# Performance work log

Measured on AMD Instinct MI355X. Metric: run time of the kernel, lower is better.

The kernel has to match this reference:

```python
import jax, jax.numpy as jnp
import numpy as np

LOD = 64          # latent observation dim
LSD = 2 * LOD     # latent state dim
BW = 3            # bandwidth
NB = 15           # num basis
B = 4096          # batch
H = 64            # hidden units of coefficient net

# band-structure indices (static, computed once)
_mask = np.triu(np.ones((LOD, LOD), np.float32), -BW) * np.tril(np.ones((LOD, LOD), np.float32), BW)
IDX0, IDX1 = np.where(_mask == 1)
DIAG_IDX = np.where(IDX0 == IDX1)[0]
NE = IDX0.shape[0]  # = 436 for lod=64, bw=3


def setup_inputs() -> dict:
    key = jax.random.key(0)
    ks = jax.random.split(key, 20)
    inp = {
        'prior_mean': jax.random.normal(ks[0], (B, LSD), jnp.float32),
        'cov_u': jax.random.uniform(ks[1], (B, LOD), jnp.float32) + 0.1,
        'cov_l': jax.random.uniform(ks[2], (B, LOD), jnp.float32) + 0.1,
        'cov_s': 0.1 * jax.random.uniform(ks[3], (B, LOD), jnp.float32),
        'obs': jax.random.normal(ks[4], (B, LOD), jnp.float32),
        'obs_var': jax.random.uniform(ks[5], (B, LOD), jnp.float32) + 0.1,
        # coefficient net params (Linear(LSD,H)-Tanh-Linear(H,H)-Tanh-Linear(H,NB)-Softmax)
        'W1': 0.05 * jax.random.normal(ks[6], (H, LSD), jnp.float32),
        'b1': jnp.zeros((H,), jnp.float32),
        'W2': 0.05 * jax.random.normal(ks[7], (H, H), jnp.float32),
        'b2': jnp.zeros((H,), jnp.float32),
        'W3': 0.05 * jax.random.normal(ks[8], (NB, H), jnp.float32),
        'b3': jnp.zeros((NB,), jnp.float32),
    }
    # transition basis matrices, flat band entries [NB, NE]
    tm11 = 0.02 * jax.random.normal(ks[9], (NB, NE), jnp.float32)
    tm12 = 0.02 * jax.random.normal(ks[10], (NB, NE), jnp.float32)
    tm12 = tm12.at[:, DIAG_IDX].add(0.2)
    tm21 = 0.02 * jax.random.normal(ks[11], (NB, NE), jnp.float32)
    tm21 = tm21.at[:, DIAG_IDX].add(-0.2)
    tm22 = 0.02 * jax.random.normal(ks[12], (NB, NE), jnp.float32)
    inp['tm11_basis'] = tm11
    inp['tm12_basis'] = tm12
    inp['tm21_basis'] = tm21
    inp['tm22_basis'] = tm22
    # log transition noise, init at var_activation_inverse(0.1) = log(exp(0.1)-1)
    inp['log_trans_noise'] = jnp.full((1, LSD), np.log(np.exp(0.1) - 1.0), jnp.float32)
    return inp


def _bmv(mat, vec):
    return jnp.einsum('bij,bj->bi', mat, vec)


def _unflatten_tm(flat):
    # flat: [B, NE] -> banded [B, LOD, LOD]
    tm = jnp.zeros((flat.shape[0], LOD, LOD), flat.dtype)
    return tm.at[:, IDX0, IDX1].set(flat)


def reference(prior_mean, cov_u, cov_l, cov_s, obs, obs_var,
              W1, b1, W2, b2, W3, b3,
              tm11_basis, tm12_basis, tm21_basis, tm22_basis, log_trans_noise):
    # ---- update (Kalman-style, factorized diagonal covariance) ----
    denom = cov_u + obs_var
    q_upper = cov_u / denom
    q_lower = cov_s / denom
    residual = obs - prior_mean[:, :LOD]
    post_mean = prior_mean + jnp.concatenate([q_upper * residual, q_lower * residual], -1)
    covar_factor = 1.0 - q_upper
    post_cu = covar_factor * cov_u
    post_cl = cov_l - q_lower * cov_s
    post_cs = covar_factor * cov_s

    # ---- coefficient net: MLP + softmax -> basis mixing coefficients ----
    h = jnp.tanh(post_mean @ W1.T + b1)
    h = jnp.tanh(h @ W2.T + b2)
    coeff = jax.nn.softmax(h @ W3.T + b3, axis=-1)  # [B, NB]

    # ---- locally-linear transition model ----
    tm11_flat = jnp.einsum('bk,ke->be', coeff, tm11_basis).at[:, DIAG_IDX].add(1.0)
    tm12_flat = jnp.einsum('bk,ke->be', coeff, tm12_basis)
    tm21_flat = jnp.einsum('bk,ke->be', coeff, tm21_basis)
    tm22_flat = jnp.einsum('bk,ke->be', coeff, tm22_basis).at[:, DIAG_IDX].add(1.0)
    tm11 = _unflatten_tm(tm11_flat)
    tm12 = _unflatten_tm(tm12_flat)
    tm21 = _unflatten_tm(tm21_flat)
    tm22 = _unflatten_tm(tm22_flat)

    trans_cov = jnp.log(jnp.exp(log_trans_noise) + 1.0)  # var_activation (softplus)
    tcu = trans_cov[:, :LOD]
    tcl = trans_cov[:, LOD:]

    # ---- predict ----
    mu = post_mean[:, :LOD]
    ml = post_mean[:, LOD:]
    next_mean = jnp.concatenate([_bmv(tm11, mu) + _bmv(tm12, ml),
                                 _bmv(tm21, mu) + _bmv(tm22, ml)], -1)
    # dadat(A, d) = bmv(A^2, d); dadbt(A, d, B) = bmv(A*B, d)
    next_cu = (_bmv(jnp.square(tm11), post_cu) + 2.0 * _bmv(tm11 * tm12, post_cs)
               + _bmv(jnp.square(tm12), post_cl) + tcu)
    next_cl = (_bmv(jnp.square(tm21), post_cu) + 2.0 * _bmv(tm21 * tm22, post_cs)
               + _bmv(jnp.square(tm22), post_cl) + tcl)
    next_cs = (_bmv(tm21 * tm11, post_cu) + _bmv(tm22 * tm11, post_cs)
               + _bmv(tm21 * tm12, post_cs) + _bmv(tm22 * tm12, post_cl))

    return (post_mean, post_cu, post_cl, post_cs, next_mean, next_cu, next_cl, next_cs)
```

## Files before the change

### kernel.cpp

```cpp
#include <hip/hip_runtime.h>
#include <math.h>

#define O_PM   0
#define O_PCU  524288
#define O_PCL  786432
#define O_PCS  1048576
#define O_NM   1310720
#define O_NCU  1835008
#define O_NCL  2097152
#define O_NCS  2359296

#define TM_S   1748
#define L_W1   0
#define L_W2   4864
#define L_W3   7680
#define L_TM   0
#define L_BAST 13984
#define L_PMB  27968
#define L_H1   29184
#define L_H2   29888
#define L_COEF 30592
#define L_PMF  30752
#define L_CUF  32800
#define L_CLF  33824
#define L_CSF  34848
#define L_TOT  35872

typedef short s8v __attribute__((ext_vector_type(8)));
typedef short s4v __attribute__((ext_vector_type(4)));
typedef float f4v __attribute__((ext_vector_type(4)));

__device__ __forceinline__ unsigned pk2(float a, float b) {
    unsigned ua = __float_as_uint(a), ub = __float_as_uint(b);
    ua += 0x7fffu + ((ua >> 16) & 1u);
    ub += 0x7fffu + ((ub >> 16) & 1u);
    return (ua >> 16) | (ub & 0xffff0000u);
}
__device__ __forceinline__ unsigned short tobf(float a) {
    unsigned ua = __float_as_uint(a);
    ua += 0x7fffu + ((ua >> 16) & 1u);
    return (unsigned short)(ua >> 16);
}
__device__ __forceinline__ float frombf(unsigned short u) {
    return __uint_as_float(((unsigned)u) << 16);
}
__device__ __forceinline__ float lo16(unsigned w) { return __uint_as_float(w << 16); }
__device__ __forceinline__ float hi16(unsigned w) { return __uint_as_float(w & 0xffff0000u); }
__device__ __forceinline__ float frcp(float x) { return __builtin_amdgcn_rcpf(x); }
__device__ __forceinline__ float ftanh(float x) {
    float e = __expf(2.f * x);
    return 1.f - 2.f * frcp(e + 1.f);
}
#define SWZ(v, imm) __uint_as_float((unsigned)__builtin_amdgcn_ds_swizzle((int)__float_as_uint(v), imm))

#if __has_builtin(__builtin_amdgcn_mfma_f32_16x16x16_bf16)
#define MFMA16(A,B,C) __builtin_amdgcn_mfma_f32_16x16x16_bf16(A,B,C,0,0,0)
#elif __has_builtin(__builtin_amdgcn_mfma_f32_16x16x16bf16_1k)
#define MFMA16(A,B,C) __builtin_amdgcn_mfma_f32_16x16x16bf16_1k(A,B,C,0,0,0)
#else
#define MFMA16(A,B,C) (C)
#endif

#if __has_builtin(__builtin_amdgcn_s_setprio)
#define SETPRIO(n) __builtin_amdgcn_s_setprio(n)
#else
#define SETPRIO(n)
#endif

__global__ __launch_bounds__(1024, 4)
void rkn_kernel(const float* __restrict__ prior_mean,
                const float* __restrict__ cov_u,
                const float* __restrict__ cov_l,
                const float* __restrict__ cov_s,
                const float* __restrict__ obs,
                const float* __restrict__ obs_var,
                const float* __restrict__ W1,
                const float* __restrict__ b1,
                const float* __restrict__ W2,
                const float* __restrict__ b2,
                const float* __restrict__ W3,
                const float* __restrict__ b3,
                const float* __restrict__ tm11b,
                const float* __restrict__ tm12b,
                const float* __restrict__ tm21b,
                const float* __restrict__ tm22b,
                const float* __restrict__ ltn,
                float* __restrict__ out)
{
    __shared__ __align__(16) unsigned smem[L_TOT];

    const int tid  = threadIdx.x;
    const int wid  = tid >> 6;
    const int lane = tid & 63;
    const int lrow = lane & 15;
    const int lkg  = lane >> 4;

    {
#pragma unroll
        for (int it = 0; it < 2; ++it) {
            const int idx = it * 1024 + tid;
            const float4 v = ((const float4*)W1)[idx];
            const int j = idx >> 5, kq = idx & 31;
            unsigned* d = smem + (L_W1 + j * 76 + kq * 2);
            d[0] = pk2(v.x, v.y); d[1] = pk2(v.z, v.w);
        }
        {
            const int idx = tid;
            const float4 v = ((const float4*)W2)[idx];
            const int j = idx >> 4, kq = idx & 15;
            unsigned* d = smem + (L_W2 + j * 44 + kq * 2);
            d[0] = pk2(v.x, v.y); d[1] = pk2(v.z, v.w);
        }
        if (tid < 240) {
            const float4 v = ((const float4*)W3)[tid];
            const int j = tid >> 4, kq = tid & 15;
            unsigned* d = smem + (L_W3 + j * 44 + kq * 2);
            d[0] = pk2(v.x, v.y); d[1] = pk2(v.z, v.w);
        } else if (tid < 284) {
            smem[L_W3 + 15 * 44 + (tid - 240)] = 0u;
        }
    }

    if (tid < 512) {
        const int prow  = tid >> 5;
        const int pd    = (tid & 31) << 1;
        const int grow1 = blockIdx.x * 16 + prow;
        const float2 cu2 = *(const float2*)(cov_u   + grow1 * 64 + pd);
        const float2 cl2 = *(const float2*)(cov_l   + grow1 * 64 + pd);
        const float2 cs2 = *(const float2*)(cov_s   + grow1 * 64 + pd);
        const float2 ob2 = *(const float2*)(obs     + grow1 * 64 + pd);
        const float2 ov2 = *(const float2*)(obs_var + grow1 * 64 + pd);
        const float2 pu2 = *(const float2*)(prior_mean + grow1 * 128 + pd);
        const float2 pl2 = *(const float2*)(prior_mean + grow1 * 128 + 64 + pd);

        const float i0 = frcp(cu2.x + ov2.x), i1 = frcp(cu2.y + ov2.y);
        const float qu0 = cu2.x * i0, qu1 = cu2.y * i1;
        const float ql0 = cs2.x * i0, ql1 = cs2.y * i1;
        const float r0 = ob2.x - pu2.x, r1 = ob2.y - pu2.y;
        const float pmu0 = pu2.x + qu0 * r0, pmu1 = pu2.y + qu1 * r1;
        const float pml0 = pl2.x + ql0 * r0, pml1 = pl2.y + ql1 * r1;
        const float cf0 = 1.f - qu0, cf1 = 1.f - qu1;
        const float pcu0 = cf0 * cu2.x, pcu1 = cf1 * cu2.y;
        const float pcl0 = cl2.x - ql0 * cs2.x, pcl1 = cl2.y - ql1 * cs2.y;
        const float pcs0 = cf0 * cs2.x, pcs1 = cf1 * cs2.y;

        *(float2*)(out + O_PM  + grow1 * 128 + pd)      = make_float2(pmu0, pmu1);
        *(float2*)(out + O_PM  + grow1 * 128 + 64 + pd) = make_float2(pml0, pml1);
        *(float2*)(out + O_PCU + grow1 * 64 + pd) = make_float2(pcu0, pcu1);
        *(float2*)(out + O_PCL + grow1 * 64 + pd) = make_float2(pcl0, pcl1);
        *(float2*)(out + O_PCS + grow1 * 64 + pd) = make_float2(pcs0, pcs1);

        smem[L_PMB + prow * 76 + (pd >> 1)]      = pk2(pmu0, pmu1);
        smem[L_PMB + prow * 76 + 32 + (pd >> 1)] = pk2(pml0, pml1);
        *(float2*)((float*)(smem + L_PMF) + prow * 128 + pd)      = make_float2(pmu0, pmu1);
        *(float2*)((float*)(smem + L_PMF) + prow * 128 + 64 + pd) = make_float2(pml0, pml1);
        *(float2*)((float*)(smem + L_CUF) + prow * 64 + pd) = make_float2(pcu0, pcu1);
        *(float2*)((float*)(smem + L_CLF) + prow * 64 + pd) = make_float2(pcl0, pcl1);
        *(float2*)((float*)(smem + L_CSF) + prow * 64 + pd) = make_float2(pcs0, pcs1);
    }

    const float tcu = __logf(__expf(ltn[lane]) + 1.f);
    const float tcl = __logf(__expf(ltn[64 + lane]) + 1.f);

    __syncthreads();

    const int t2 = tid - 256;
    const int ms = t2 & 3;
    const float* bps = (ms == 0) ? tm11b : (ms == 1) ? tm12b : (ms == 2) ? tm21b : tm22b;

    if (wid < 4) {
        SETPRIO(1);
        const int w = wid;
        f4v acc = {0.f, 0.f, 0.f, 0.f};
#pragma unroll
        for (int s = 0; s < 4; ++s) {
            s8v a = *(const s8v*)(smem + L_PMB + lrow * 76 + s * 16 + lkg * 4);
            s8v b = *(const s8v*)(smem + L_W1 + (w * 16 + lrow) * 76 + s * 16 + lkg * 4);
            acc = __builtin_amdgcn_mfma_f32_16x16x32_bf16(a, b, acc, 0, 0, 0);
        }
        const float bc1 = b1[w * 16 + lrow];
        unsigned short* h1u = (unsigned short*)(smem + L_H1);
#pragma unroll
        for (int q = 0; q < 4; ++q)
            h1u[(lkg * 4 + q) * 88 + w * 16 + lrow] = tobf(ftanh(acc[q] + bc1));
        SETPRIO(0);
    } else {
#pragma unroll
        for (int kp = 0; kp < 3; ++kp)
#pragma unroll
            for (int c = 0; c < 3; ++c) {
                const int n = c * 768 + t2;
                if (n < 1744) {
                    const int e = n >> 2;
                    const float lo = bps[(2 * kp) * 436 + e];
                    const float hi = bps[(2 * kp + 1) * 436 + e];
                    smem[L_BAST + kp * TM_S + n] = pk2(lo, hi);
                }
            }
    }
    __syncthreads();

    if (wid < 4) {
        SETPRIO(1);
        const int w = wid;
        f4v acc = {0.f, 0.f, 0.f, 0.f};
#pragma unroll
        for (int s = 0; s < 2; ++s) {
            s8v a = *(const s8v*)(smem + L_H1 + lrow * 44 + s * 16 + lkg * 4);
            s8v b = *(const s8v*)(smem + L_W2 + (w * 16 + lrow) * 44 + s * 16 + lkg * 4);
            acc = __builtin_amdgcn_mfma_f32_16x16x32_bf16(a, b, acc, 0, 0, 0);
        }
        const float bc2 = b2[w * 16 + lrow];
        unsigned short* h2u = (unsigned short*)(smem + L_H2);
#pragma unroll
        for (int q = 0; q < 4; ++q)
            h2u[(lkg * 4 + q) * 88 + w * 16 + lrow] = tobf(ftanh(acc[q] + bc2));
        SETPRIO(0);
    } else {
#pragma unroll
        for (int kp = 3; kp < 6; ++kp)
#pragma unroll
            for (int c = 0; c < 3; ++c) {
                const int n = c * 768 + t2;
                if (n < 1744) {
                    const int e = n >> 2;
                    const float lo = bps[(2 * kp) * 436 + e];
                    const float hi = bps[(2 * kp + 1) * 436 + e];
                    smem[L_BAST + kp * TM_S + n] = pk2(lo, hi);
                }
            }
    }
    __syncthreads();

    if (wid == 0) {
        SETPRIO(1);
        f4v acc = {0.f, 0.f, 0.f, 0.f};
#pragma unroll
        for (int s = 0; s < 2; ++s) {
            s8v a = *(const s8v*)(smem + L_H2 + lrow * 44 + s * 16 + lkg * 4);
            s8v b = *(const s8v*)(smem + L_W3 + lrow * 44 + s * 16 + lkg * 4);
            acc = __builtin_amdgcn_mfma_f32_16x16x32_bf16(a, b, acc, 0, 0, 0);
        }
        const float bc3 = (lrow < 15) ? b3[lrow] : 0.f;
        unsigned short* cfu = (unsigned short*)(smem + L_COEF);
#pragma unroll
        for (int q = 0; q < 4; ++q) {
            const float lg = acc[q] + bc3;
            float v = (lrow < 15) ? lg : -1e30f;
            v = fmaxf(v, SWZ(v, 0x041F));
            v = fmaxf(v, SWZ(v, 0x081F));
            v = fmaxf(v, SWZ(v, 0x101F));
            v = fmaxf(v, SWZ(v, 0x201F));
            const float ex = (lrow < 15) ? __expf(lg - v) : 0.f;
            float ss = ex;
            ss += SWZ(ss, 0x041F);
            ss += SWZ(ss, 0x081F);
            ss += SWZ(ss, 0x101F);
            ss += SWZ(ss, 0x201F);
            cfu[(lkg * 4 + q) * 20 + lrow] = tobf(ex * frcp(ss));
        }
        SETPRIO(0);
    } else if (wid >= 4) {
#pragma unroll
        for (int kp = 6; kp < 8; ++kp)
#pragma unroll
            for (int c = 0; c < 3; ++c) {
                const int n = c * 768 + t2;
                if (n < 1744) {
                    const int e = n >> 2;
                    const float lo = bps[(2 * kp) * 436 + e];
                    const float hi = (kp < 7) ? bps[(2 * kp + 1) * 436 + e] : 0.f;
                    smem[L_BAST + kp * TM_S + n] = pk2(lo, hi);
                }
            }
    }
    __syncthreads();

    {
        unsigned short* tmu = (unsigned short*)(smem + L_TM);
        const s4v ca = *(const s4v*)(smem + L_COEF + lrow * 10 + lkg * 2);
#pragma unroll
        for (int i = 0; i < 7; ++i) {
            const int t = i * 16 + wid;
            if (t < 109) {
                const int nn = t * 16 + lrow;
                unsigned wpair[2];
                wpair[0] = smem[L_BAST + (lkg * 2    ) * TM_S + nn];
                wpair[1] = smem[L_BAST + (lkg * 2 + 1) * TM_S + nn];
                const s4v bb = *(const s4v*)wpair;
                f4v d = {0.f, 0.f, 0.f, 0.f};
                d = MFMA16(ca, bb, d);
#pragma unroll
                for (int q = 0; q < 4; ++q)
                    tmu[(lkg * 4 + q) * TM_S + nn] = tobf(d[q]);
            }
        }
    }
    __syncthreads();

    {
        const int i   = lane;
        const int jlo = (i - 3 > 0) ? (i - 3) : 0;
        const int ne  = ((i + 3 < 63) ? (i + 3) : 63) - jlo + 1;
        const int base = (i < 4)  ? (i * (i + 7)) / 2
                       : (i <= 61) ? (7 * i - 6)
                       : (i == 62) ? 427 : 432;
        const float* pmf = (const float*)(smem + L_PMF);
        const float* cuf = (const float*)(smem + L_CUF);
        const float* clf = (const float*)(smem + L_CLF);
        const float* csf = (const float*)(smem + L_CSF);
        const uint2* tmr = (const uint2*)smem;

        const int r  = wid;
        const int gr = blockIdx.x * 16 + r;
        float nmu = 0.f, nml = 0.f, ncu = 0.f, ncl = 0.f, ncs = 0.f;
#pragma unroll
        for (int dd = 0; dd < 7; ++dd) {
            if (dd < ne) {
                const int j = jlo + dd;
                const uint2 tv = tmr[r * (TM_S / 4) + base + dd];
                float t11 = lo16(tv.x);
                float t12 = hi16(tv.x);
                float t21 = lo16(tv.y);
                float t22 = hi16(tv.y);
                if (j == i) { t11 += 1.f; t22 += 1.f; }
                const float mu  = pmf[r * 128 + j];
                const float ml  = pmf[r * 128 + 64 + j];
                const float vcu = cuf[r * 64 + j];
                const float vcl = clf[r * 64 + j];
                const float vcs = csf[r * 64 + j];
                nmu += t11 * mu + t12 * ml;
                nml += t21 * mu + t22 * ml;
                ncu += t11 * t11 * vcu + 2.f * t11 * t12 * vcs + t12 * t12 * vcl;
                ncl += t21 * t21 * vcu + 2.f * t21 * t22 * vcs + t22 * t22 * vcl;
                ncs += t21 * t11 * vcu + (t22 * t11 + t21 * t12) * vcs + t22 * t12 * vcl;
            }
        }
        out[O_NM  + gr * 128 + i]      = nmu;
        out[O_NM  + gr * 128 + 64 + i] = nml;
        out[O_NCU + gr * 64 + i] = ncu + tcu;
        out[O_NCL + gr * 64 + i] = ncl + tcl;
        out[O_NCS + gr * 64 + i] = ncs;
    }
}

extern "C" void kernel_launch(void* const* d_in, const int* in_sizes, int n_in,
                              void* d_out, int out_size, void* d_ws, size_t ws_size,
                              hipStream_t stream) {
    rkn_kernel<<<dim3(256), dim3(1024), 0, stream>>>(
        (const float*)d_in[0],
        (const float*)d_in[1],
        (const float*)d_in[2],
        (const float*)d_in[3],
        (const float*)d_in[4],
        (const float*)d_in[5],
        (const float*)d_in[6],
        (const float*)d_in[7],
        (const float*)d_in[8],
        (const float*)d_in[9],
        (const float*)d_in[10],
        (const float*)d_in[11],
        (const float*)d_in[12],
        (const float*)d_in[13],
        (const float*)d_in[14],
        (const float*)d_in[15],
        (const float*)d_in[16],
        (float*)d_out);
}
```

Baseline: 16.77 us.

## Compute full coefficient MLP redundantly per wave to remove block barriers

Each of the four MLP waves now computes all hidden-layer tiles and the softmax on its own, using a private LDS scratch area, so the two intermediate __syncthreads between layers are gone. The basis-packing waves handle all eight kp slices in one loop while the MLP runs. This trades four times the MFMA work in the MLP for fewer block-wide barriers and a longer stretch of overlap with the packing waves. Only wave 0 writes the coefficients, so the other three waves' work is redundant.

New measurement: 16.75 us. About the same (-0.1%).

```diff
diff --git a/kernel.cpp b/kernel.cpp
--- a/kernel.cpp
+++ b/kernel.cpp
@@ -17,14 +17,13 @@
 #define L_TM   0
 #define L_BAST 13984
 #define L_PMB  27968
-#define L_H1   29184
-#define L_H2   29888
-#define L_COEF 30592
-#define L_PMF  30752
-#define L_CUF  32800
-#define L_CLF  33824
-#define L_CSF  34848
-#define L_TOT  35872
+#define L_HP   29184
+#define L_COEF 33792
+#define L_PMF  33952
+#define L_CUF  36000
+#define L_CLF  37024
+#define L_CSF  38048
+#define L_TOT  39072
 
 typedef short s8v __attribute__((ext_vector_type(8)));
 typedef short s4v __attribute__((ext_vector_type(4)));
@@ -170,99 +169,69 @@
 
     if (wid < 4) {
         SETPRIO(1);
-        const int w = wid;
-        f4v acc = {0.f, 0.f, 0.f, 0.f};
-#pragma unroll
-        for (int s = 0; s < 4; ++s) {
-            s8v a = *(const s8v*)(smem + L_PMB + lrow * 76 + s * 16 + lkg * 4);
-            s8v b = *(const s8v*)(smem + L_W1 + (w * 16 + lrow) * 76 + s * 16 + lkg * 4);
-            acc = __builtin_amdgcn_mfma_f32_16x16x32_bf16(a, b, acc, 0, 0, 0);
-        }
-        const float bc1 = b1[w * 16 + lrow];
-        unsigned short* h1u = (unsigned short*)(smem + L_H1);
-#pragma unroll
-        for (int q = 0; q < 4; ++q)
-            h1u[(lkg * 4 + q) * 88 + w * 16 + lrow] = tobf(ftanh(acc[q] + bc1));
+        unsigned short* h1p = (unsigned short*)(smem + L_HP + wid * 1152);
+        unsigned short* h2p = (unsigned short*)(smem + L_HP + wid * 1152 + 576);
+
+#pragma unroll
+        for (int ct = 0; ct < 4; ++ct) {
+            f4v acc = {0.f, 0.f, 0.f, 0.f};
+#pragma unroll
+            for (int s = 0; s < 4; ++s) {
+                s8v a = *(const s8v*)(smem + L_PMB + lrow * 76 + s * 16 + lkg * 4);
+                s8v b = *(const s8v*)(smem + L_W1 + (ct * 16 + lrow) * 76 + s * 16 + lkg * 4);
+                acc = __builtin_amdgcn_mfma_f32_16x16x32_bf16(a, b, acc, 0, 0, 0);
+            }
+            const float bc = b1[ct * 16 + lrow];
+#pragma unroll
+            for (int q = 0; q < 4; ++q)
+                h1p[(lkg * 4 + q) * 72 + ct * 16 + lrow] = tobf(ftanh(acc[q] + bc));
+        }
+#pragma unroll
+        for (int ct = 0; ct < 4; ++ct) {
+            f4v acc = {0.f, 0.f, 0.f, 0.f};
+#pragma unroll
+            for (int s = 0; s < 2; ++s) {
+                s8v a = *(const s8v*)(h1p + lrow * 72 + s * 32 + lkg * 8);
+                s8v b = *(const s8v*)(smem + L_W2 + (ct * 16 + lrow) * 44 + s * 16 + lkg * 4);
+                acc = __builtin_amdgcn_mfma_f32_16x16x32_bf16(a, b, acc, 0, 0, 0);
+            }
+            const float bc = b2[ct * 16 + lrow];
+#pragma unroll
+            for (int q = 0; q < 4; ++q)
+                h2p[(lkg * 4 + q) * 72 + ct * 16 + lrow] = tobf(ftanh(acc[q] + bc));
+        }
+        {
+            f4v acc = {0.f, 0.f, 0.f, 0.f};
+#pragma unroll
+            for (int s = 0; s < 2; ++s) {
+                s8v a = *(const s8v*)(h2p + lrow * 72 + s * 32 + lkg * 8);
+                s8v b = *(const s8v*)(smem + L_W3 + lrow * 44 + s * 16 + lkg * 4);
+                acc = __builtin_amdgcn_mfma_f32_16x16x32_bf16(a, b, acc, 0, 0, 0);
+            }
+            const float bc3 = (lrow < 15) ? b3[lrow] : 0.f;
+            unsigned short* cfu = (unsigned short*)(smem + L_COEF);
+#pragma unroll
+            for (int q = 0; q < 4; ++q) {
+                const float lg = acc[q] + bc3;
+                float v = (lrow < 15) ? lg : -1e30f;
+                v = fmaxf(v, SWZ(v, 0x041F));
+                v = fmaxf(v, SWZ(v, 0x081F));
+                v = fmaxf(v, SWZ(v, 0x101F));
+                v = fmaxf(v, SWZ(v, 0x201F));
+                const float ex = (lrow < 15) ? __expf(lg - v) : 0.f;
+                float ss = ex;
+                ss += SWZ(ss, 0x041F);
+                ss += SWZ(ss, 0x081F);
+                ss += SWZ(ss, 0x101F);
+                ss += SWZ(ss, 0x201F);
+                if (wid == 0)
+                    cfu[(lkg * 4 + q) * 20 + lrow] = tobf(ex * frcp(ss));
+            }
+        }
         SETPRIO(0);
     } else {
 #pragma unroll
-        for (int kp = 0; kp < 3; ++kp)
-#pragma unroll
-            for (int c = 0; c < 3; ++c) {
-                const int n = c * 768 + t2;
-                if (n < 1744) {
-                    const int e = n >> 2;
-                    const float lo = bps[(2 * kp) * 436 + e];
-                    const float hi = bps[(2 * kp + 1) * 436 + e];
-                    smem[L_BAST + kp * TM_S + n] = pk2(lo, hi);
-                }
-            }
-    }
-    __syncthreads();
-
-    if (wid < 4) {
-        SETPRIO(1);
-        const int w = wid;
-        f4v acc = {0.f, 0.f, 0.f, 0.f};
-#pragma unroll
-        for (int s = 0; s < 2; ++s) {
-            s8v a = *(const s8v*)(smem + L_H1 + lrow * 44 + s * 16 + lkg * 4);
-            s8v b = *(const s8v*)(smem + L_W2 + (w * 16 + lrow) * 44 + s * 16 + lkg * 4);
-            acc = __builtin_amdgcn_mfma_f32_16x16x32_bf16(a, b, acc, 0, 0, 0);
-        }
-        const float bc2 = b2[w * 16 + lrow];
-        unsigned short* h2u = (unsigned short*)(smem + L_H2);
-#pragma unroll
-        for (int q = 0; q < 4; ++q)
-            h2u[(lkg * 4 + q) * 88 + w * 16 + lrow] = tobf(ftanh(acc[q] + bc2));
-        SETPRIO(0);
-    } else {
-#pragma unroll
-        for (int kp = 3; kp < 6; ++kp)
-#pragma unroll
-            for (int c = 0; c < 3; ++c) {
-                const int n = c * 768 + t2;
-                if (n < 1744) {
-                    const int e = n >> 2;
-                    const float lo = bps[(2 * kp) * 436 + e];
-                    const float hi = bps[(2 * kp + 1) * 436 + e];
-                    smem[L_BAST + kp * TM_S + n] = pk2(lo, hi);
-                }
-            }
-    }
-    __syncthreads();
-
-    if (wid == 0) {
-        SETPRIO(1);
-        f4v acc = {0.f, 0.f, 0.f, 0.f};
-#pragma unroll
-        for (int s = 0; s < 2; ++s) {
-            s8v a = *(const s8v*)(smem + L_H2 + lrow * 44 + s * 16 + lkg * 4);
-            s8v b = *(const s8v*)(smem + L_W3 + lrow * 44 + s * 16 + lkg * 4);
-            acc = __builtin_amdgcn_mfma_f32_16x16x32_bf16(a, b, acc, 0, 0, 0);
-        }
-        const float bc3 = (lrow < 15) ? b3[lrow] : 0.f;
-        unsigned short* cfu = (unsigned short*)(smem + L_COEF);
-#pragma unroll
-        for (int q = 0; q < 4; ++q) {
-            const float lg = acc[q] + bc3;
-            float v = (lrow < 15) ? lg : -1e30f;
-            v = fmaxf(v, SWZ(v, 0x041F));
-            v = fmaxf(v, SWZ(v, 0x081F));
-            v = fmaxf(v, SWZ(v, 0x101F));
-            v = fmaxf(v, SWZ(v, 0x201F));
-            const float ex = (lrow < 15) ? __expf(lg - v) : 0.f;
-            float ss = ex;
-            ss += SWZ(ss, 0x041F);
-            ss += SWZ(ss, 0x081F);
-            ss += SWZ(ss, 0x101F);
-            ss += SWZ(ss, 0x201F);
-            cfu[(lkg * 4 + q) * 20 + lrow] = tobf(ex * frcp(ss));
-        }
-        SETPRIO(0);
-    } else if (wid >= 4) {
-#pragma unroll
-        for (int kp = 6; kp < 8; ++kp)
+        for (int kp = 0; kp < 8; ++kp)
 #pragma unroll
             for (int c = 0; c < 3; ++c) {
                 const int n = c * 768 + t2;
```
